# Kernel tuning notes

Measured on AMD Instinct MI355X. Metric: run time of the kernel, lower is better.

The kernel has to match this reference:

```python
import jax, jax.numpy as jnp
import numpy as np

L, H, P = 16384, 1024, 512
DT_MIN, DT_MAX = 1e-3, 1e-1
STEP_RESCALE = 1.0


def setup_inputs() -> dict:
    key = jax.random.key(0)
    ks = jax.random.split(key, 7)
    input_sequence = jax.random.normal(ks[0], (L, H), jnp.float32)
    # eigenvalues with negative real part (left half plane), HiPPO-like imag parts
    Lambda_re = -(jax.random.uniform(ks[1], (P,), jnp.float32) * 0.9 + 0.1)
    Lambda_im = jnp.pi * jnp.arange(P, dtype=jnp.float32)
    B = jax.random.normal(ks[2], (P, H, 2), jnp.float32) / jnp.sqrt(2.0 * H)   # real/imag of B_tilde (P,H)
    C = jax.random.normal(ks[3], (H, P, 2), jnp.float32) / jnp.sqrt(2.0 * P)   # real/imag of C_tilde (H,P)
    D = jax.random.normal(ks[4], (H,), jnp.float32)
    u01 = jax.random.uniform(ks[5], (P, 1), jnp.float32)
    log_step = jnp.log(DT_MIN) + u01 * (jnp.log(DT_MAX) - jnp.log(DT_MIN))     # (P,1)
    return dict(input_sequence=input_sequence, Lambda_re=Lambda_re, Lambda_im=Lambda_im,
                B=B, C=C, D=D, log_step=log_step)


def _binop(q_i, q_j):
    # diagonal linear recurrence composition: (A, b) pairs
    A_i, b_i = q_i
    A_j, b_j = q_j
    return A_j * A_i, A_j * b_i + b_j


def reference(input_sequence, Lambda_re, Lambda_im, B, C, D, log_step):
    Lambda = Lambda_re + 1j * Lambda_im                        # (P,) complex64
    B_tilde = B[..., 0] + 1j * B[..., 1]                       # (P,H)
    C_tilde = C[..., 0] + 1j * C[..., 1]                       # (H,P)
    step = STEP_RESCALE * jnp.exp(log_step[:, 0])              # (P,)
    # ZOH discretization
    Lambda_bar = jnp.exp(Lambda * step)                        # (P,)
    B_bar = ((Lambda_bar - 1.0) / Lambda)[:, None] * B_tilde   # (P,H)
    # Bu_elements: (L,P) complex
    Bu = input_sequence.astype(B_bar.dtype) @ B_bar.T
    Lambda_elems = jnp.broadcast_to(Lambda_bar, Bu.shape)      # (L,P)
    # parallel associative scan over the diagonal recurrence x_t = Lambda_bar*x_{t-1} + Bu_t
    _, xs = jax.lax.associative_scan(_binop, (Lambda_elems, Bu))
    ys = 2.0 * (xs @ C_tilde.T).real                           # conj_sym => factor 2, (L,H)
    return ys + D * input_sequence
```

## Files before the change

### kernel.cpp

```cpp
#include <hip/hip_runtime.h>
#include <math.h>

#define L_SEQ 16384
#define H_DIM 1024
#define P_DIM 512
#define N2P   1024
#define KDIM  1024
#define NTILE 16
#define CHUNK 64
#define NCHUNK 256

typedef __attribute__((ext_vector_type(8))) short short8;
typedef __attribute__((ext_vector_type(4))) float f32x4;

__device__ __forceinline__ unsigned short f2bf(float f){
    unsigned int u = __float_as_uint(f);
    u = (u + 0x7FFFu + ((u >> 16) & 1u)) >> 16;
    return (unsigned short)u;
}

__global__ void k_prep_lambda(const float* __restrict__ lre, const float* __restrict__ lim,
                              const float* __restrict__ lstep,
                              float* __restrict__ lam, float* __restrict__ coef,
                              float* __restrict__ lpow)
{
    int p = threadIdx.x;
    double step = exp((double)lstep[p]);
    double dr = (double)lre[p], di = (double)lim[p];
    double ar = dr*step, ai = di*step;
    double er = exp(ar);
    double lbr = er*cos(ai), lbi = er*sin(ai);
    lam[2*p] = (float)lbr; lam[2*p+1] = (float)lbi;
    double nr = lbr - 1.0, ni = lbi;
    double d2 = dr*dr + di*di;
    coef[2*p]   = (float)((nr*dr + ni*di)/d2);
    coef[2*p+1] = (float)((ni*dr - nr*di)/d2);
    double xr = lbr, xi = lbi;
    #pragma unroll
    for (int s=0;s<6;s++){ double t = xr*xr - xi*xi; xi = 2.0*xr*xi; xr = t; }
    lpow[2*p] = (float)xr; lpow[2*p+1] = (float)xi;
}

__global__ __launch_bounds__(256)
void k_prep_BB(const float* __restrict__ B, const float* __restrict__ coef,
               unsigned short* __restrict__ BB)
{
    int i = blockIdx.x*256 + threadIdx.x;
    int p = i >> 10, h = i & 1023;
    float br = B[2*i], bi = B[2*i+1];
    float cr = coef[2*p], ci = coef[2*p+1];
    BB[(size_t)(2*p)*H_DIM + h]   = f2bf(cr*br - ci*bi);
    BB[(size_t)(2*p+1)*H_DIM + h] = f2bf(cr*bi + ci*br);
}

__global__ __launch_bounds__(256)
void k_prep_CC(const float* __restrict__ C, unsigned short* __restrict__ CC)
{
    int i = blockIdx.x*256 + threadIdx.x;
    int h = i >> 9, p = i & 511;
    float cr = C[2*i], ci = C[2*i+1];
    CC[(size_t)h*N2P + 2*p]     = f2bf(2.f*cr);
    CC[(size_t)h*N2P + 2*p + 1] = f2bf(-2.f*ci);
}

__global__ __launch_bounds__(256)
void k_cast(const float4* __restrict__ u, unsigned short* __restrict__ o)
{
    int i = blockIdx.x*256 + threadIdx.x;
    float4 a = u[2*i], b = u[2*i+1];
    union { short8 v; unsigned short s[8]; } r;
    r.s[0]=f2bf(a.x); r.s[1]=f2bf(a.y); r.s[2]=f2bf(a.z); r.s[3]=f2bf(a.w);
    r.s[4]=f2bf(b.x); r.s[5]=f2bf(b.y); r.s[6]=f2bf(b.z); r.s[7]=f2bf(b.w);
    *reinterpret_cast<short8*>(o + (size_t)i*8) = r.v;
}

template<int EPI>
__global__ __launch_bounds__(512, 2)
void gemm256(const unsigned short* __restrict__ A, const unsigned short* __restrict__ Bm,
             float* __restrict__ Cc, const float* __restrict__ Dv, const float* __restrict__ U)
{
    __shared__ char lds[131072];
    const int tid  = threadIdx.x;
    const int lane = tid & 63;
    const int wid  = tid >> 6;
    const int wm = wid >> 2, wn = wid & 3;
    const int wg = ((int)blockIdx.x & 7) * 32 + ((int)blockIdx.x >> 3);
    const int tm = wg >> 2, tn = wg & 3;

    const int lr = lane & 15;
    const int l8 = lane >> 3;
    const int i0 = wid * 8 + l8;
    const int scol = ((lane & 7) * 8) ^ ((l8 & 7) << 3);
    const int kc0 = ( (lane >> 4) * 16      ) ^ ((lr & 7) << 4);
    const int kc1 = ( (lane >> 4) * 16 + 64 ) ^ ((lr & 7) << 4);
    const int aBase = wm * 8192 + lr * 128;
    const int bBase = 32768 + wn * 4096 + lr * 128;
    const int ldsW = wid * 1024;

    const size_t arow0 = (size_t)(tm*256 + i0) * KDIM + scol;
    const int rb0 = ((i0 >> 5) << 6) | (i0 & 31);
    const size_t brow0 = (size_t)(tn*256 + rb0) * KDIM + scol;

#define GLOAD(SRC, DST) __builtin_amdgcn_global_load_lds( \
        (const __attribute__((address_space(1))) void*)(SRC), \
        (__attribute__((address_space(3))) void*)(DST), 16, 0, 0)
#define STAGE_A(g, tt, sbN) do{ \
    const unsigned short* s_ = A + arow0 + (size_t)(g)*64*KDIM + (size_t)(tt)*64; \
    GLOAD(s_,                    lds + (sbN) + (g)*16384 + ldsW); \
    GLOAD(s_ + (size_t)128*KDIM, lds + (sbN) + (g)*16384 + 8192 + ldsW); \
  }while(0)
#define STAGE_B(g, tt, sbN) do{ \
    const unsigned short* s_ = Bm + brow0 + (size_t)(g)*32*KDIM + (size_t)(tt)*64; \
    GLOAD(s_,                    lds + (sbN) + 32768 + (g)*16384 + ldsW); \
    GLOAD(s_ + (size_t)128*KDIM, lds + (sbN) + 32768 + (g)*16384 + 8192 + ldsW); \
  }while(0)
#define RD(OFF) (*(const short8*)(lds + (OFF)))
#define MFMA(a,b,c) __builtin_amdgcn_mfma_f32_16x16x32_bf16(a,b,c,0,0,0)
#define VMW6 asm volatile("s_waitcnt vmcnt(6)" ::: "memory")
#define BAR __builtin_amdgcn_s_barrier()

    short8 af[4][2], b0[2][2], b1[2][2];
    f32x4 acc[8][4];
    #pragma unroll
    for (int m=0;m<8;m++)
        #pragma unroll
        for (int n=0;n<4;n++) acc[m][n] = (f32x4){0.f,0.f,0.f,0.f};

    STAGE_A(0, 0, 0); STAGE_B(0, 0, 0); STAGE_B(1, 0, 0); STAGE_A(1, 0, 0);

    for (int t = 0; t < NTILE; ++t) {
        const int sb  = (t & 1) << 16;
        const int sbN = sb ^ 65536;
        const int tt  = (t+1 < NTILE) ? t+1 : t;
        STAGE_A(0, tt, sbN);
        VMW6; BAR;
        #pragma unroll
        for (int m=0;m<4;m++){ af[m][0]=RD(sb+aBase+m*2048+kc0); af[m][1]=RD(sb+aBase+m*2048+kc1); }
        #pragma unroll
        for (int n=0;n<2;n++){ b0[n][0]=RD(sb+bBase+n*2048+kc0); b0[n][1]=RD(sb+bBase+n*2048+kc1); }
        __builtin_amdgcn_s_setprio(1);
        #pragma unroll
        for (int m=0;m<4;m++)
            #pragma unroll
            for (int n=0;n<2;n++){
                acc[m][n]=MFMA(af[m][0],b0[n][0],acc[m][n]);
                acc[m][n]=MFMA(af[m][1],b0[n][1],acc[m][n]); }
        __builtin_amdgcn_s_setprio(0); BAR;
        STAGE_B(0, tt, sbN);
        VMW6; BAR;
        #pragma unroll
        for (int n=0;n<2;n++){ b1[n][0]=RD(sb+bBase+16384+n*2048+kc0); b1[n][1]=RD(sb+bBase+16384+n*2048+kc1); }
        __builtin_amdgcn_s_setprio(1);
        #pragma unroll
        for (int m=0;m<4;m++)
            #pragma unroll
            for (int n=0;n<2;n++){
                acc[m][2+n]=MFMA(af[m][0],b1[n][0],acc[m][2+n]);
                acc[m][2+n]=MFMA(af[m][1],b1[n][1],acc[m][2+n]); }
        __builtin_amdgcn_s_setprio(0); BAR;
        STAGE_B(1, tt, sbN);
        VMW6; BAR;
        #pragma unroll
        for (int m=0;m<4;m++){ af[m][0]=RD(sb+16384+aBase+m*2048+kc0); af[m][1]=RD(sb+16384+aBase+m*2048+kc1); }
        __builtin_amdgcn_s_setprio(1);
        #pragma unroll
        for (int m=0;m<4;m++)
            #pragma unroll
            for (int n=0;n<2;n++){
                acc[4+m][n]=MFMA(af[m][0],b0[n][0],acc[4+m][n]);
                acc[4+m][n]=MFMA(af[m][1],b0[n][1],acc[4+m][n]); }
        __builtin_amdgcn_s_setprio(0); BAR;
        STAGE_A(1, tt, sbN);
        BAR;
        __builtin_amdgcn_s_setprio(1);
        #pragma unroll
        for (int m=0;m<4;m++)
            #pragma unroll
            for (int n=0;n<2;n++){
                acc[4+m][2+n]=MFMA(af[m][0],b1[n][0],acc[4+m][2+n]);
                acc[4+m][2+n]=MFMA(af[m][1],b1[n][1],acc[4+m][2+n]); }
        __builtin_amdgcn_s_setprio(0); BAR;
    }
    asm volatile("s_waitcnt vmcnt(0)" ::: "memory");

    const int orow0 = tm*256 + wm*128 + (lane>>4)*4;
    const int ocol0 = tn*256 + wn*64 + lr;
    #pragma unroll
    for (int m=0;m<8;m++){
        #pragma unroll
        for (int n=0;n<4;n++){
            int row = orow0 + m*16, col = ocol0 + n*16;
            #pragma unroll
            for (int j=0;j<4;j++){
                size_t idx = (size_t)(row + j)*N2P + col;
                float v = acc[m][n][j];
                if (EPI) v += Dv[col]*U[idx];
                Cc[idx] = v;
            }
        }
    }
#undef GLOAD
#undef STAGE_A
#undef STAGE_B
#undef RD
#undef MFMA
#undef VMW6
#undef BAR
}

__global__ __launch_bounds__(512)
void k_agg(const float* __restrict__ Bu, const float* __restrict__ lam, float* __restrict__ agg)
{
    int p = threadIdx.x, c = blockIdx.x;
    float lrr = lam[2*p], lii = lam[2*p+1];
    float xr = 0.f, xi = 0.f;
    const float2* b2 = (const float2*)Bu + (size_t)c*CHUNK*512 + p;
    #pragma unroll 4
    for (int t=0;t<CHUNK;t++){
        float2 b = b2[(size_t)t*512];
        float tr = lrr*xr - lii*xi + b.x;
        xi = lrr*xi + lii*xr + b.y;
        xr = tr;
    }
    agg[((size_t)c*P_DIM + p)*2]     = xr;
    agg[((size_t)c*P_DIM + p)*2 + 1] = xi;
}

__global__ __launch_bounds__(256)
void k_scan(const float* __restrict__ agg, const float* __restrict__ lpow,
            float* __restrict__ xinit)
{
    __shared__ float sr[NCHUNK], si[NCHUNK];
    int c = threadIdx.x, p = blockIdx.x;
    float xr = agg[((size_t)c*P_DIM + p)*2];
    float xi = agg[((size_t)c*P_DIM + p)*2 + 1];
    sr[c] = xr; si[c] = xi;
    float wr = lpow[2*p], wi = lpow[2*p+1];
    for (int s=1; s<NCHUNK; s<<=1){
        __syncthreads();
        float ur = 0.f, ui = 0.f;
        if (c >= s){ ur = sr[c-s]; ui = si[c-s]; }
        __syncthreads();
        xr += wr*ur - wi*ui;
        xi += wr*ui + wi*ur;
        sr[c] = xr; si[c] = xi;
        float t = wr*wr - wi*wi; wi = 2.f*wr*wi; wr = t;
    }
    __syncthreads();
    float er = 0.f, ei = 0.f;
    if (c > 0){ er = sr[c-1]; ei = si[c-1]; }
    xinit[((size_t)c*P_DIM + p)*2]     = er;
    xinit[((size_t)c*P_DIM + p)*2 + 1] = ei;
}

__global__ __launch_bounds__(512)
void k_apply(const float* __restrict__ Bu, const float* __restrict__ lam,
             const float* __restrict__ xinit, unsigned int* __restrict__ xs)
{
    int p = threadIdx.x, c = blockIdx.x;
    float lrr = lam[2*p], lii = lam[2*p+1];
    float xr = xinit[((size_t)c*P_DIM + p)*2];
    float xi = xinit[((size_t)c*P_DIM + p)*2 + 1];
    const float2* b2 = (const float2*)Bu + (size_t)c*CHUNK*512 + p;
    unsigned int* o = xs + (size_t)c*CHUNK*512 + p;
    #pragma unroll 4
    for (int t=0;t<CHUNK;t++){
        float2 b = b2[(size_t)t*512];
        float tr = lrr*xr - lii*xi + b.x;
        xi = lrr*xi + lii*xr + b.y;
        xr = tr;
        o[(size_t)t*512] = (unsigned int)f2bf(xr) | ((unsigned int)f2bf(xi) << 16);
    }
}

extern "C" void kernel_launch(void* const* d_in, const int* in_sizes, int n_in,
                              void* d_out, int out_size, void* d_ws, size_t ws_size,
                              hipStream_t stream)
{
    const float* u   = (const float*)d_in[0];
    const float* lre = (const float*)d_in[1];
    const float* lim = (const float*)d_in[2];
    const float* B   = (const float*)d_in[3];
    const float* C   = (const float*)d_in[4];
    const float* D   = (const float*)d_in[5];
    const float* ls  = (const float*)d_in[6];
    float* out = (float*)d_out;

    char* w = (char*)d_ws;
    unsigned short* u16  = (unsigned short*)(w + 0);
    unsigned short* xs16 = (unsigned short*)(w + 33554432);
    unsigned short* BB   = (unsigned short*)(w + 67108864);
    unsigned short* CC   = (unsigned short*)(w + 69206016);
    float* lam   = (float*)(w + 71303168);
    float* coef  = (float*)(w + 71307264);
    float* lpow  = (float*)(w + 71311360);
    float* agg   = (float*)(w + 71315456);
    float* xinit = (float*)(w + 72364032);

    k_prep_lambda<<<1, P_DIM, 0, stream>>>(lre, lim, ls, lam, coef, lpow);
    k_prep_BB<<<(P_DIM*H_DIM)/256, 256, 0, stream>>>(B, coef, BB);
    k_prep_CC<<<(H_DIM*P_DIM)/256, 256, 0, stream>>>(C, CC);
    k_cast<<<(L_SEQ*H_DIM)/(256*8), 256, 0, stream>>>((const float4*)u, u16);

    gemm256<0><<<256, 512, 0, stream>>>(u16, BB, out, nullptr, nullptr);

    k_agg<<<NCHUNK, P_DIM, 0, stream>>>(out, lam, agg);
    k_scan<<<P_DIM, NCHUNK, 0, stream>>>(agg, lpow, xinit);
    k_apply<<<NCHUNK, P_DIM, 0, stream>>>(out, lam, xinit, (unsigned int*)xs16);

    gemm256<1><<<256, 512, 0, stream>>>(xs16, CC, out, D, u);
}
```

Measured before the change: 147.8 us.

## Store Bu in bf16, use bf16 input for D term, restructure GEMM pipeline

After: 135.9 us. -8.1%, faster.

```diff
diff --git a/kernel.cpp b/kernel.cpp
--- a/kernel.cpp
+++ b/kernel.cpp
@@ -6,7 +6,7 @@
 #define P_DIM 512
 #define N2P   1024
 #define KDIM  1024
-#define NTILE 16
+#define NTILE 32
 #define CHUNK 64
 #define NCHUNK 256
 
@@ -17,6 +17,9 @@
     unsigned int u = __float_as_uint(f);
     u = (u + 0x7FFFu + ((u >> 16) & 1u)) >> 16;
     return (unsigned short)u;
+}
+__device__ __forceinline__ float bf2f(unsigned int lo16){
+    return __uint_as_float(lo16 << 16);
 }
 
 __global__ void k_prep_lambda(const float* __restrict__ lre, const float* __restrict__ lim,
@@ -77,7 +80,8 @@
 template<int EPI>
 __global__ __launch_bounds__(512, 2)
 void gemm256(const unsigned short* __restrict__ A, const unsigned short* __restrict__ Bm,
-             float* __restrict__ Cc, const float* __restrict__ Dv, const float* __restrict__ U)
+             float* __restrict__ Cf, unsigned short* __restrict__ Cb,
+             const float* __restrict__ Dv, const unsigned short* __restrict__ U16)
 {
     __shared__ char lds[131072];
     const int tid  = threadIdx.x;
@@ -86,100 +90,70 @@
     const int wm = wid >> 2, wn = wid & 3;
     const int wg = ((int)blockIdx.x & 7) * 32 + ((int)blockIdx.x >> 3);
     const int tm = wg >> 2, tn = wg & 3;
-
     const int lr = lane & 15;
-    const int l8 = lane >> 3;
-    const int i0 = wid * 8 + l8;
-    const int scol = ((lane & 7) * 8) ^ ((l8 & 7) << 3);
-    const int kc0 = ( (lane >> 4) * 16      ) ^ ((lr & 7) << 4);
-    const int kc1 = ( (lane >> 4) * 16 + 64 ) ^ ((lr & 7) << 4);
-    const int aBase = wm * 8192 + lr * 128;
-    const int bBase = 32768 + wn * 4096 + lr * 128;
+
+    const int srow = wid*16 + (lane >> 2);
+    const int scol = (((lane & 3) ^ ((lane >> 2) & 3)) << 3);
+    const size_t aS0 = (size_t)(tm*256 + srow) * KDIM + scol;
+    const size_t bS0 = (size_t)(tn*256 + srow) * KDIM + scol;
     const int ldsW = wid * 1024;
 
-    const size_t arow0 = (size_t)(tm*256 + i0) * KDIM + scol;
-    const int rb0 = ((i0 >> 5) << 6) | (i0 & 31);
-    const size_t brow0 = (size_t)(tn*256 + rb0) * KDIM + scol;
+    const int kc   = (((lane >> 4) << 4) ^ ((lr & 3) << 4));
+    const int aOff = (wm*128 + lr)*64 + kc;
+    const int bOff = 65536 + (wn*64 + lr)*64 + kc;
 
 #define GLOAD(SRC, DST) __builtin_amdgcn_global_load_lds( \
         (const __attribute__((address_space(1))) void*)(SRC), \
         (__attribute__((address_space(3))) void*)(DST), 16, 0, 0)
-#define STAGE_A(g, tt, sbN) do{ \
-    const unsigned short* s_ = A + arow0 + (size_t)(g)*64*KDIM + (size_t)(tt)*64; \
-    GLOAD(s_,                    lds + (sbN) + (g)*16384 + ldsW); \
-    GLOAD(s_ + (size_t)128*KDIM, lds + (sbN) + (g)*16384 + 8192 + ldsW); \
-  }while(0)
-#define STAGE_B(g, tt, sbN) do{ \
-    const unsigned short* s_ = Bm + brow0 + (size_t)(g)*32*KDIM + (size_t)(tt)*64; \
-    GLOAD(s_,                    lds + (sbN) + 32768 + (g)*16384 + ldsW); \
-    GLOAD(s_ + (size_t)128*KDIM, lds + (sbN) + 32768 + (g)*16384 + 8192 + ldsW); \
-  }while(0)
+#define STAGE_A(tt) do{ int bb_ = ((tt)&3)*16384; \
+    const unsigned short* s_ = A + aS0 + (size_t)(tt)*32; \
+    GLOAD(s_,                    lds + bb_ + ldsW); \
+    GLOAD(s_ + (size_t)128*KDIM, lds + bb_ + 8192 + ldsW); }while(0)
+#define STAGE_B(tt) do{ int bb_ = 65536 + ((tt)&3)*16384; \
+    const unsigned short* s_ = Bm + bS0 + (size_t)(tt)*32; \
+    GLOAD(s_,                    lds + bb_ + ldsW); \
+    GLOAD(s_ + (size_t)128*KDIM, lds + bb_ + 8192 + ldsW); }while(0)
 #define RD(OFF) (*(const short8*)(lds + (OFF)))
 #define MFMA(a,b,c) __builtin_amdgcn_mfma_f32_16x16x32_bf16(a,b,c,0,0,0)
-#define VMW6 asm volatile("s_waitcnt vmcnt(6)" ::: "memory")
 #define BAR __builtin_amdgcn_s_barrier()
 
-    short8 af[4][2], b0[2][2], b1[2][2];
+    short8 af[8], bfr[4];
     f32x4 acc[8][4];
     #pragma unroll
     for (int m=0;m<8;m++)
         #pragma unroll
         for (int n=0;n<4;n++) acc[m][n] = (f32x4){0.f,0.f,0.f,0.f};
 
-    STAGE_A(0, 0, 0); STAGE_B(0, 0, 0); STAGE_B(1, 0, 0); STAGE_A(1, 0, 0);
+    STAGE_A(0); STAGE_B(0); STAGE_A(1); STAGE_B(1); STAGE_A(2); STAGE_B(2);
 
     for (int t = 0; t < NTILE; ++t) {
-        const int sb  = (t & 1) << 16;
-        const int sbN = sb ^ 65536;
-        const int tt  = (t+1 < NTILE) ? t+1 : t;
-        STAGE_A(0, tt, sbN);
-        VMW6; BAR;
-        #pragma unroll
-        for (int m=0;m<4;m++){ af[m][0]=RD(sb+aBase+m*2048+kc0); af[m][1]=RD(sb+aBase+m*2048+kc1); }
-        #pragma unroll
-        for (int n=0;n<2;n++){ b0[n][0]=RD(sb+bBase+n*2048+kc0); b0[n][1]=RD(sb+bBase+n*2048+kc1); }
+        const int sb = (t & 3) * 16384;
+        const int tt = (t+3 < NTILE) ? t+3 : NTILE-1;
+        STAGE_A(tt);
+        asm volatile("s_waitcnt vmcnt(10)" ::: "memory");
+        BAR;
+        #pragma unroll
+        for (int m=0;m<8;m++) af[m] = RD(sb + aOff + m*1024);
+        bfr[0] = RD(sb + bOff);
+        bfr[1] = RD(sb + bOff + 1024);
         __builtin_amdgcn_s_setprio(1);
         #pragma unroll
-        for (int m=0;m<4;m++)
-            #pragma unroll
-            for (int n=0;n<2;n++){
-                acc[m][n]=MFMA(af[m][0],b0[n][0],acc[m][n]);
-                acc[m][n]=MFMA(af[m][1],b0[n][1],acc[m][n]); }
-        __builtin_amdgcn_s_setprio(0); BAR;
-        STAGE_B(0, tt, sbN);
-        VMW6; BAR;
-        #pragma unroll
-        for (int n=0;n<2;n++){ b1[n][0]=RD(sb+bBase+16384+n*2048+kc0); b1[n][1]=RD(sb+bBase+16384+n*2048+kc1); }
+        for (int m=0;m<8;m++){
+            acc[m][0] = MFMA(af[m], bfr[0], acc[m][0]);
+            acc[m][1] = MFMA(af[m], bfr[1], acc[m][1]);
+        }
+        __builtin_amdgcn_s_setprio(0);
+        STAGE_B(tt);
+        BAR;
+        bfr[2] = RD(sb + bOff + 2048);
+        bfr[3] = RD(sb + bOff + 3072);
         __builtin_amdgcn_s_setprio(1);
         #pragma unroll
-        for (int m=0;m<4;m++)
-            #pragma unroll
-            for (int n=0;n<2;n++){
-                acc[m][2+n]=MFMA(af[m][0],b1[n][0],acc[m][2+n]);
-                acc[m][2+n]=MFMA(af[m][1],b1[n][1],acc[m][2+n]); }
-        __builtin_amdgcn_s_setprio(0); BAR;
-        STAGE_B(1, tt, sbN);
-        VMW6; BAR;
-        #pragma unroll
-        for (int m=0;m<4;m++){ af[m][0]=RD(sb+16384+aBase+m*2048+kc0); af[m][1]=RD(sb+16384+aBase+m*2048+kc1); }
-        __builtin_amdgcn_s_setprio(1);
-        #pragma unroll
-        for (int m=0;m<4;m++)
-            #pragma unroll
-            for (int n=0;n<2;n++){
-                acc[4+m][n]=MFMA(af[m][0],b0[n][0],acc[4+m][n]);
-                acc[4+m][n]=MFMA(af[m][1],b0[n][1],acc[4+m][n]); }
-        __builtin_amdgcn_s_setprio(0); BAR;
-        STAGE_A(1, tt, sbN);
-        BAR;
-        __builtin_amdgcn_s_setprio(1);
-        #pragma unroll
-        for (int m=0;m<4;m++)
-            #pragma unroll
-            for (int n=0;n<2;n++){
-                acc[4+m][2+n]=MFMA(af[m][0],b1[n][0],acc[4+m][2+n]);
-                acc[4+m][2+n]=MFMA(af[m][1],b1[n][1],acc[4+m][2+n]); }
-        __builtin_amdgcn_s_setprio(0); BAR;
+        for (int m=0;m<8;m++){
+            acc[m][2] = MFMA(af[m], bfr[2], acc[m][2]);
+            acc[m][3] = MFMA(af[m], bfr[3], acc[m][3]);
+        }
+        __builtin_amdgcn_s_setprio(0);
     }
     asm volatile("s_waitcnt vmcnt(0)" ::: "memory");
 
@@ -193,9 +167,8 @@
             #pragma unroll
             for (int j=0;j<4;j++){
                 size_t idx = (size_t)(row + j)*N2P + col;
-                float v = acc[m][n][j];
-                if (EPI) v += Dv[col]*U[idx];
-                Cc[idx] = v;
+                if (EPI) Cf[idx] = acc[m][n][j] + Dv[col]*bf2f(U16[idx]);
+                else     Cb[idx] = f2bf(acc[m][n][j]);
             }
         }
     }
@@ -204,22 +177,24 @@
 #undef STAGE_B
 #undef RD
 #undef MFMA
-#undef VMW6
 #undef BAR
 }
 
 __global__ __launch_bounds__(512)
-void k_agg(const float* __restrict__ Bu, const float* __restrict__ lam, float* __restrict__ agg)
+void k_agg(const unsigned int* __restrict__ Bu, const float* __restrict__ lam,
+           float* __restrict__ agg)
 {
     int p = threadIdx.x, c = blockIdx.x;
     float lrr = lam[2*p], lii = lam[2*p+1];
     float xr = 0.f, xi = 0.f;
-    const float2* b2 = (const float2*)Bu + (size_t)c*CHUNK*512 + p;
+    const unsigned int* b2 = Bu + (size_t)c*CHUNK*512 + p;
     #pragma unroll 4
     for (int t=0;t<CHUNK;t++){
-        float2 b = b2[(size_t)t*512];
-        float tr = lrr*xr - lii*xi + b.x;
-        xi = lrr*xi + lii*xr + b.y;
+        unsigned int b = b2[(size_t)t*512];
+        float br = __uint_as_float(b << 16);
+        float bi = __uint_as_float(b & 0xffff0000u);
+        float tr = lrr*xr - lii*xi + br;
+        xi = lrr*xi + lii*xr + bi;
         xr = tr;
     }
     agg[((size_t)c*P_DIM + p)*2]     = xr;
@@ -254,20 +229,22 @@
 }
 
 __global__ __launch_bounds__(512)
-void k_apply(const float* __restrict__ Bu, const float* __restrict__ lam,
+void k_apply(const unsigned int* __restrict__ Bu, const float* __restrict__ lam,
              const float* __restrict__ xinit, unsigned int* __restrict__ xs)
 {
     int p = threadIdx.x, c = blockIdx.x;
     float lrr = lam[2*p], lii = lam[2*p+1];
     float xr = xinit[((size_t)c*P_DIM + p)*2];
     float xi = xinit[((size_t)c*P_DIM + p)*2 + 1];
-    const float2* b2 = (const float2*)Bu + (size_t)c*CHUNK*512 + p;
+    const unsigned int* b2 = Bu + (size_t)c*CHUNK*512 + p;
     unsigned int* o = xs + (size_t)c*CHUNK*512 + p;
     #pragma unroll 4
     for (int t=0;t<CHUNK;t++){
-        float2 b = b2[(size_t)t*512];
-        float tr = lrr*xr - lii*xi + b.x;
-        xi = lrr*xi + lii*xr + b.y;
+        unsigned int b = b2[(size_t)t*512];
+        float br = __uint_as_float(b << 16);
+        float bi = __uint_as_float(b & 0xffff0000u);
+        float tr = lrr*xr - lii*xi + br;
+        xi = lrr*xi + lii*xr + bi;
         xr = tr;
         o[(size_t)t*512] = (unsigned int)f2bf(xr) | ((unsigned int)f2bf(xi) << 16);
     }
@@ -289,24 +266,26 @@
     char* w = (char*)d_ws;
     unsigned short* u16  = (unsigned short*)(w + 0);
     unsigned short* xs16 = (unsigned short*)(w + 33554432);
-    unsigned short* BB   = (unsigned short*)(w + 67108864);
-    unsigned short* CC   = (unsigned short*)(w + 69206016);
-    float* lam   = (float*)(w + 71303168);
-    float* coef  = (float*)(w + 71307264);
-    float* lpow  = (float*)(w + 71311360);
-    float* agg   = (float*)(w + 71315456);
-    float* xinit = (float*)(w + 72364032);
+    unsigned short* Bu16 = (unsigned short*)(w + 67108864);
+    unsigned short* BB   = (unsigned short*)(w + 100663296);
+    unsigned short* CC   = (unsigned short*)(w + 102760448);
+    float* lam   = (float*)(w + 104857600);
+    float* coef  = (float*)(w + 104861696);
+    float* lpow  = (float*)(w + 104865792);
+    float* agg   = (float*)(w + 104869888);
+    float* xinit = (float*)(w + 105918464);
 
     k_prep_lambda<<<1, P_DIM, 0, stream>>>(lre, lim, ls, lam, coef, lpow);
     k_prep_BB<<<(P_DIM*H_DIM)/256, 256, 0, stream>>>(B, coef, BB);
     k_prep_CC<<<(H_DIM*P_DIM)/256, 256, 0, stream>>>(C, CC);
     k_cast<<<(L_SEQ*H_DIM)/(256*8), 256, 0, stream>>>((const float4*)u, u16);
 
-    gemm256<0><<<256, 512, 0, stream>>>(u16, BB, out, nullptr, nullptr);
-
-    k_agg<<<NCHUNK, P_DIM, 0, stream>>>(out, lam, agg);
+    gemm256<0><<<256, 512, 0, stream>>>(u16, BB, nullptr, Bu16, nullptr, nullptr);
+
+    k_agg<<<NCHUNK, P_DIM, 0, stream>>>((const unsigned int*)Bu16, lam, agg);
     k_scan<<<P_DIM, NCHUNK, 0, stream>>>(agg, lpow, xinit);
-    k_apply<<<NCHUNK, P_DIM, 0, stream>>>(out, lam, xinit, (unsigned int*)xs16);
-
-    gemm256<1><<<256, 512, 0, stream>>>(xs16, CC, out, D, u);
-}
+    k_apply<<<NCHUNK, P_DIM, 0, stream>>>((const unsigned int*)Bu16, lam, xinit,
+                                          (unsigned int*)xs16);
+
+    gemm256<1><<<256, 512, 0, stream>>>(xs16, CC, out, nullptr, D, u16);
+}
```
